# Kernel optimization log

Measured on AMD Instinct MI355X. Metric: run time of the kernel, lower is better.

Reference implementation:

```python
import jax, jax.numpy as jnp
import numpy as np

TEMPERATURE = 0.07
BASE_TEMPERATURE = 0.07


def setup_inputs() -> dict:
    key = jax.random.key(0)
    k1, k2 = jax.random.split(key)
    N, D = 8192, 512
    features = jax.random.normal(k1, (N, D), dtype=jnp.float32)
    labels = jax.random.randint(k2, (N,), 0, 64, dtype=jnp.int64 if jax.config.jax_enable_x64 else jnp.int32)
    return {"features": features, "labels": labels, "rotation_multiplier": 2}


def reference(features, labels, rotation_multiplier):
    k = int(rotation_multiplier)
    N = features.shape[0]
    B = N // k
    # L2-normalize rows (torch F.normalize clamps norm at eps=1e-12)
    norm = jnp.maximum(jnp.linalg.norm(features, axis=1, keepdims=True), 1e-12)
    f = features / norm
    sim = jnp.matmul(f, f.T) / TEMPERATURE  # [N, N]

    # block positive mask: groups of k rows share a label; compare group labels
    lab = labels.reshape(B, k)[:, 0]  # [B]
    same = lab[:, None] == lab[None, :]  # [B, B]
    mask = jnp.repeat(jnp.repeat(same, k, axis=0), k, axis=1)  # [N, N]
    eye = jnp.eye(N, dtype=bool)
    mask = mask & ~eye

    # stable masked log-softmax with diagonal removed from denominator
    logits_max = jax.lax.stop_gradient(jnp.max(sim, axis=1, keepdims=True))
    logits = sim - logits_max
    exp_logits = jnp.exp(logits)
    denom = exp_logits.sum(axis=1, keepdims=True) - jnp.diagonal(exp_logits)[:, None] + 1e-8
    log_prob = logits - jnp.log(denom)

    mask_f = mask.astype(logits.dtype)
    mask_sum = mask_f.sum(axis=1)  # [N]
    valid = mask_sum > 0
    mean_log_prob_pos = (log_prob * mask_f).sum(axis=1) / jnp.maximum(mask_sum, 1.0)
    per_sample = -(TEMPERATURE / BASE_TEMPERATURE) * mean_log_prob_pos
    n_valid = valid.sum().astype(logits.dtype)
    loss = jnp.where(valid, per_sample, 0.0).sum() / jnp.maximum(n_valid, 1.0)
    return loss
```

## Files before the change

### kernel.cpp

```cpp
#include <hip/hip_runtime.h>
#include <hip/hip_bf16.h>

#define TEMP_INV 14.285714285714286f
#define FSCALE 16.0f
#define T1S (TEMP_INV / 256.0f)

typedef __attribute__((ext_vector_type(4))) float f32x4;
typedef __attribute__((ext_vector_type(4))) int i32x4;
typedef __attribute__((ext_vector_type(8))) int i32x8;

#define ASYNC_COPY16(gp, lp)                                                  \
  __builtin_amdgcn_global_load_lds(                                          \
      (__attribute__((address_space(1))) const void*)(gp),                    \
      (__attribute__((address_space(3))) void*)(lp), 16, 0, 0)

__global__ __launch_bounds__(256) void norm_k(const float* __restrict__ feat,
                                              uchar* __restrict__ fq,
                                              const int* __restrict__ labels,
                                              const int* __restrict__ kptr,
                                              int* __restrict__ glab,
                                              float* __restrict__ gacc,
                                              int* __restrict__ dcnt,
                                              int N, int D) {
  const int row = (blockIdx.x * 256 + threadIdx.x) >> 6;
  const int lane = threadIdx.x & 63;
  if (row < N) {
    const float4* fr = (const float4*)(feat + (size_t)row * D);
    float4 v0 = fr[lane * 2];
    float4 v1 = fr[lane * 2 + 1];
    float ss = v0.x * v0.x + v0.y * v0.y + v0.z * v0.z + v0.w * v0.w +
               v1.x * v1.x + v1.y * v1.y + v1.z * v1.z + v1.w * v1.w;
    #pragma unroll
    for (int off = 32; off; off >>= 1) ss += __shfl_xor(ss, off, 64);
    const float inv = FSCALE / fmaxf(sqrtf(ss), 1e-12f);
    int w0 = 0, w1 = 0;
    w0 = __builtin_amdgcn_cvt_pk_fp8_f32(v0.x * inv, v0.y * inv, w0, false);
    w0 = __builtin_amdgcn_cvt_pk_fp8_f32(v0.z * inv, v0.w * inv, w0, true);
    w1 = __builtin_amdgcn_cvt_pk_fp8_f32(v1.x * inv, v1.y * inv, w1, false);
    w1 = __builtin_amdgcn_cvt_pk_fp8_f32(v1.z * inv, v1.w * inv, w1, true);
    uint2 o; o.x = (uint)w0; o.y = (uint)w1;
    const int pofs = (lane >> 4) * 128 + (lane & 3) * 32 + ((lane >> 2) & 3) * 8;
    *(uint2*)(fq + (size_t)row * D + pofs) = o;
    if (lane == 0) {
      const int k = *kptr;
      glab[row] = labels[(size_t)(row / k) * k];
    }
  }
  if (blockIdx.x == 0 && threadIdx.x < 3) {
    if (threadIdx.x < 2) gacc[threadIdx.x] = 0.f;
    else *dcnt = 0;
  }
}

__global__ __launch_bounds__(256, 4) void gemm_k(const uchar* __restrict__ fq,
                                                 const int* __restrict__ glab,
                                                 float* __restrict__ part,
                                                 int N, int D) {
  __shared__ uchar As[128 * 128];
  __shared__ uchar Bs[128 * 128];
  const int t = threadIdx.x;
  const int lane = t & 63;
  const int wid = t >> 6;
  const int wrow = wid >> 1, wcol = wid & 1;
  const int quad = lane >> 4, l15 = lane & 15;

  const int nb = N / 128;
  const int total = nb * (nb + 1) / 2;
  int gidx = blockIdx.x;
  if ((total & 7) == 0) {
    const int per = total >> 3;
    gidx = (blockIdx.x & 7) * per + (blockIdx.x >> 3);
  }
  int idx = gidx, bi = 0;
  while (idx >= nb - bi) { idx -= nb - bi; bi++; }
  const int bj = bi + idx;
  const int i0 = bi * 128, j0 = bj * 128;
  const bool diagblk = (bi == bj);

  f32x4 acc[4][4];
  #pragma unroll
  for (int mi = 0; mi < 4; mi++)
    #pragma unroll
    for (int ni = 0; ni < 4; ni++) {
      f32x4 z = {0.f, 0.f, 0.f, 0.f};
      acc[mi][ni] = z;
    }

  uchar* sb = (wid < 2) ? As : Bs;
  const int rbase = (wid & 1) * 64;
  const int rowstart = ((wid < 2) ? i0 : j0) + rbase;
  const int lrow = lane >> 3;
  const int lch = lane & 7;

  for (int kb = 0; kb < D; kb += 128) {
    __syncthreads();
    #pragma unroll
    for (int i = 0; i < 8; i++) {
      const int rl = 8 * i + lrow;
      const int cg = lch ^ (rl & 7);
      ASYNC_COPY16(fq + (size_t)(rowstart + rl) * D + kb + cg * 16,
                   sb + (rbase + 8 * i) * 128);
    }
    __syncthreads();
    i32x8 av[4];
    #pragma unroll
    for (int mi = 0; mi < 4; mi++) {
      const int r = wrow * 64 + mi * 16 + l15;
      i32x4 lo = *(const i32x4*)&As[r * 128 + (((2 * quad) ^ (r & 7)) << 4)];
      i32x4 hi = *(const i32x4*)&As[r * 128 + (((2 * quad + 1) ^ (r & 7)) << 4)];
      av[mi] = (i32x8){lo.x, lo.y, lo.z, lo.w, hi.x, hi.y, hi.z, hi.w};
    }
    #pragma unroll
    for (int ni = 0; ni < 4; ni++) {
      const int r = wcol * 64 + ni * 16 + l15;
      i32x4 lo = *(const i32x4*)&Bs[r * 128 + (((2 * quad) ^ (r & 7)) << 4)];
      i32x4 hi = *(const i32x4*)&Bs[r * 128 + (((2 * quad + 1) ^ (r & 7)) << 4)];
      i32x8 bv = (i32x8){lo.x, lo.y, lo.z, lo.w, hi.x, hi.y, hi.z, hi.w};
      #pragma unroll
      for (int mi = 0; mi < 4; mi++)
        acc[mi][ni] = __builtin_amdgcn_mfma_scale_f32_16x16x128_f8f6f4(
            av[mi], bv, acc[mi][ni], 0, 0, 0, 127, 0, 127);
    }
  }

  __syncthreads();
  float* sf = (float*)As;
  const int colbase = j0 + wcol * 64 + l15;
  int clab[4];
  #pragma unroll
  for (int ni = 0; ni < 4; ni++) clab[ni] = glab[colbase + ni * 16];

  float colE[4] = {0.f, 0.f, 0.f, 0.f};
  float colP[4] = {0.f, 0.f, 0.f, 0.f};

  #pragma unroll
  for (int mi = 0; mi < 4; mi++) {
    const int lrw = wrow * 64 + mi * 16 + quad * 4;
    #pragma unroll
    for (int r = 0; r < 4; r++) {
      const int row = i0 + lrw + r;
      const int rlab = glab[row];
      float Ssum = 0.f, Psum = 0.f;
      #pragma unroll
      for (int ni = 0; ni < 4; ni++) {
        const int col = colbase + ni * 16;
        const float val = acc[mi][ni][r];
        const float lg = fmaf(val, T1S, -TEMP_INV);
        const bool diag = diagblk && (row == col);
        const float e = diag ? 0.f : __expf(lg);
        const float pm = (!diag && rlab == clab[ni]) ? lg : 0.f;
        Ssum += e; Psum += pm;
        colE[ni] += e; colP[ni] += pm;
      }
      #pragma unroll
      for (int off = 8; off; off >>= 1) {
        Ssum += __shfl_xor(Ssum, off, 64);
        Psum += __shfl_xor(Psum, off, 64);
      }
      if (l15 == 0) {
        sf[wcol * 128 + lrw + r]       = Ssum;
        sf[256 + wcol * 128 + lrw + r] = Psum;
      }
    }
  }
  if (!diagblk) {
    #pragma unroll
    for (int ni = 0; ni < 4; ni++) {
      float e = colE[ni];
      float p = colP[ni];
      e += __shfl_xor(e, 16, 64);
      e += __shfl_xor(e, 32, 64);
      p += __shfl_xor(p, 16, 64);
      p += __shfl_xor(p, 32, 64);
      const int lcol = wcol * 64 + ni * 16 + l15;
      if (quad == 0) {
        sf[512 + wrow * 128 + lcol] = e;
        sf[768 + wrow * 128 + lcol] = p;
      }
    }
  }
  __syncthreads();
  float* dst = part + (size_t)gidx * 512;
  if (t < 128) {
    dst[t]       = sf[t] + sf[128 + t];
    dst[128 + t] = sf[256 + t] + sf[384 + t];
  } else if (!diagblk) {
    const int u = t - 128;
    dst[256 + u] = sf[512 + u] + sf[640 + u];
    dst[384 + u] = sf[768 + u] + sf[896 + u];
  }
}

__global__ __launch_bounds__(1024) void reduce_loss_k(const float* __restrict__ part,
                                                      const int* __restrict__ glab,
                                                      const int* __restrict__ labels,
                                                      const int* __restrict__ kptr,
                                                      float* __restrict__ gacc,
                                                      int* __restrict__ dcnt,
                                                      float* __restrict__ out, int N) {
  const int nb = N / 128;
  const int b = blockIdx.x;
  const int tt = threadIdx.x;
  const int t = tt & 127;
  const int sl = tt >> 7;
  const int k = *kptr;
  const int B = N / k;

  __shared__ int h[64];
  if (tt < 64) h[tt] = 0;
  __syncthreads();
  for (int g = tt; g < B; g += 1024) {
    int lb = labels[(size_t)g * k];
    if (lb >= 0 && lb < 64) atomicAdd(&h[lb], 1);
  }

  float S = 0.f, P = 0.f;
  const int base = b * nb - b * (b - 1) / 2;
  for (int bj = b + sl; bj < nb; bj += 8) {
    const float* p = part + (size_t)(base + bj - b) * 512;
    S += p[t];
    P += p[128 + t];
  }
  for (int bi = sl; bi < b; bi += 8) {
    const int idx = bi * nb - bi * (bi - 1) / 2 + (b - bi);
    const float* p = part + (size_t)idx * 512;
    S += p[256 + t];
    P += p[384 + t];
  }
  __shared__ float sS[8][128], sP[8][128];
  sS[sl][t] = S; sP[sl][t] = P;
  __syncthreads();
  float l = 0.f, v = 0.f;
  if (sl == 0) {
    S = 0.f; P = 0.f;
    #pragma unroll
    for (int s = 0; s < 8; s++) { S += sS[s][t]; P += sP[s][t]; }
    const int np = h[glab[b * 128 + t]] * k - 1;
    if (np > 0) {
      l = -(P - (float)np * logf(S + 1e-8f)) / (float)np;
      v = 1.f;
    }
  }
  #pragma unroll
  for (int off = 32; off; off >>= 1) {
    l += __shfl_xor(l, off, 64);
    v += __shfl_xor(v, off, 64);
  }
  __shared__ float sl16[16], sv16[16];
  if ((tt & 63) == 0) { sl16[tt >> 6] = l; sv16[tt >> 6] = v; }
  __syncthreads();
  if (tt == 0) {
    float L = 0.f, V = 0.f;
    #pragma unroll
    for (int i = 0; i < 16; i++) { L += sl16[i]; V += sv16[i]; }
    atomicAdd(&gacc[0], L);
    atomicAdd(&gacc[1], V);
    __threadfence();
    const int prev = atomicAdd(dcnt, 1);
    if (prev == (int)gridDim.x - 1) {
      const float Lf = atomicAdd(&gacc[0], 0.f);
      const float Vf = atomicAdd(&gacc[1], 0.f);
      out[0] = Lf / fmaxf(Vf, 1.f);
    }
  }
}

extern "C" void kernel_launch(void* const* d_in, const int* in_sizes, int n_in,
                              void* d_out, int out_size, void* d_ws, size_t ws_size,
                              hipStream_t stream) {
  const float* feat = (const float*)d_in[0];
  const int* labels = (const int*)d_in[1];
  const int* kptr   = (const int*)d_in[2];
  const int N = in_sizes[1];
  const int D = in_sizes[0] / N;

  const int nb = N / 128;
  const int total = nb * (nb + 1) / 2;

  char* ws = (char*)d_ws;
  uchar* fq = (uchar*)ws;
  size_t off = (size_t)N * D;
  float* part = (float*)(ws + off); off += (size_t)total * 512 * sizeof(float);
  int* glab   = (int*)(ws + off);   off += (size_t)N * sizeof(int);
  float* gacc = (float*)(ws + off); off += 2 * sizeof(float);
  int* dcnt   = (int*)(ws + off);   off += sizeof(int);

  norm_k<<<(N + 3) / 4, 256, 0, stream>>>(feat, fq, labels, kptr, glab,
                                          gacc, dcnt, N, D);
  gemm_k<<<total, 256, 0, stream>>>(fq, glab, part, N, D);
  reduce_loss_k<<<nb, 1024, 0, stream>>>(part, glab, labels, kptr, gacc, dcnt,
                                         (float*)d_out, N);
}
```

Measured before the change: 128.7 us.

## Double-buffer LDS tiles in the FP8 GEMM to overlap loads with MFMA

The single As/Bs LDS tiles become double buffers, and the next K-slice is prefetched with async global-to-LDS copies while the current slice is consumed. Manual vmcnt waits and raw barriers replace the two __syncthreads per iteration, and s_setprio raises wave priority around the MFMA block. This is meant to hide global load latency behind matrix math. It doubles LDS use to 64KB per block and drops the launch-bounds occupancy hint from 4 to 2 blocks per CU, which reduces latency hiding across blocks.

```diff
diff --git a/kernel.cpp b/kernel.cpp
--- a/kernel.cpp
+++ b/kernel.cpp
@@ -52,12 +52,12 @@
   }
 }
 
-__global__ __launch_bounds__(256, 4) void gemm_k(const uchar* __restrict__ fq,
+__global__ __launch_bounds__(256, 2) void gemm_k(const uchar* __restrict__ fq,
                                                  const int* __restrict__ glab,
                                                  float* __restrict__ part,
                                                  int N, int D) {
-  __shared__ uchar As[128 * 128];
-  __shared__ uchar Bs[128 * 128];
+  __shared__ uchar As[2][128 * 128];
+  __shared__ uchar Bs[2][128 * 128];
   const int t = threadIdx.x;
   const int lane = t & 63;
   const int wid = t >> 6;
@@ -86,44 +86,59 @@
       acc[mi][ni] = z;
     }
 
-  uchar* sb = (wid < 2) ? As : Bs;
   const int rbase = (wid & 1) * 64;
   const int rowstart = ((wid < 2) ? i0 : j0) + rbase;
   const int lrow = lane >> 3;
   const int lch = lane & 7;
-
-  for (int kb = 0; kb < D; kb += 128) {
-    __syncthreads();
+  const uchar* gsrc = fq + (size_t)rowstart * D;
+
+  auto STAGE = [&](int buf, int kbyte) {
+    uchar* sb = (wid < 2) ? As[buf] : Bs[buf];
     #pragma unroll
     for (int i = 0; i < 8; i++) {
       const int rl = 8 * i + lrow;
       const int cg = lch ^ (rl & 7);
-      ASYNC_COPY16(fq + (size_t)(rowstart + rl) * D + kb + cg * 16,
+      ASYNC_COPY16(gsrc + (size_t)rl * D + kbyte + cg * 16,
                    sb + (rbase + 8 * i) * 128);
     }
-    __syncthreads();
+  };
+
+  const int nk = D >> 7;
+  STAGE(0, 0);
+  for (int kt = 0; kt < nk; kt++) {
+    const int cur = kt & 1;
+    if (kt + 1 < nk) {
+      STAGE(cur ^ 1, (kt + 1) << 7);
+      asm volatile("s_waitcnt vmcnt(8)" ::: "memory");
+    } else {
+      asm volatile("s_waitcnt vmcnt(0)" ::: "memory");
+    }
+    asm volatile("s_barrier" ::: "memory");
+
     i32x8 av[4];
     #pragma unroll
     for (int mi = 0; mi < 4; mi++) {
       const int r = wrow * 64 + mi * 16 + l15;
-      i32x4 lo = *(const i32x4*)&As[r * 128 + (((2 * quad) ^ (r & 7)) << 4)];
-      i32x4 hi = *(const i32x4*)&As[r * 128 + (((2 * quad + 1) ^ (r & 7)) << 4)];
+      i32x4 lo = *(const i32x4*)&As[cur][r * 128 + (((2 * quad) ^ (r & 7)) << 4)];
+      i32x4 hi = *(const i32x4*)&As[cur][r * 128 + (((2 * quad + 1) ^ (r & 7)) << 4)];
       av[mi] = (i32x8){lo.x, lo.y, lo.z, lo.w, hi.x, hi.y, hi.z, hi.w};
     }
+    __builtin_amdgcn_s_setprio(1);
     #pragma unroll
     for (int ni = 0; ni < 4; ni++) {
       const int r = wcol * 64 + ni * 16 + l15;
-      i32x4 lo = *(const i32x4*)&Bs[r * 128 + (((2 * quad) ^ (r & 7)) << 4)];
-      i32x4 hi = *(const i32x4*)&Bs[r * 128 + (((2 * quad + 1) ^ (r & 7)) << 4)];
+      i32x4 lo = *(const i32x4*)&Bs[cur][r * 128 + (((2 * quad) ^ (r & 7)) << 4)];
+      i32x4 hi = *(const i32x4*)&Bs[cur][r * 128 + (((2 * quad + 1) ^ (r & 7)) << 4)];
       i32x8 bv = (i32x8){lo.x, lo.y, lo.z, lo.w, hi.x, hi.y, hi.z, hi.w};
       #pragma unroll
       for (int mi = 0; mi < 4; mi++)
         acc[mi][ni] = __builtin_amdgcn_mfma_scale_f32_16x16x128_f8f6f4(
             av[mi], bv, acc[mi][ni], 0, 0, 0, 127, 0, 127);
     }
-  }
-
-  __syncthreads();
+    __builtin_amdgcn_s_setprio(0);
+    asm volatile("s_barrier" ::: "memory");
+  }
+
   float* sf = (float*)As;
   const int colbase = j0 + wcol * 64 + l15;
   int clab[4];
```

Measured after the change: 130.7 us. About the same (+1.6%).

## Load FP8 MFMA operands directly from global memory, dropping LDS staging

Applied to the files above, without the earlier changes.

The GEMM no longer stages A and B tiles in LDS through async global-to-LDS copies with barriers. Each wave now reads its MFMA operand fragments straight from global memory, relying on cache for reuse, and fully unrolls the K loop when D is 512. LDS shrinks to a small float scratch for the epilogue and launch bounds drop to 2 blocks per CU, giving more registers. The cost is redundant global and L2 traffic, since waves sharing rows each fetch their own copy, and the loads become uncoalesced 16-byte row fragments.

```diff
diff --git a/kernel.cpp b/kernel.cpp
--- a/kernel.cpp
+++ b/kernel.cpp
@@ -8,11 +8,6 @@
 typedef __attribute__((ext_vector_type(4))) float f32x4;
 typedef __attribute__((ext_vector_type(4))) int i32x4;
 typedef __attribute__((ext_vector_type(8))) int i32x8;
-
-#define ASYNC_COPY16(gp, lp)                                                  \
-  __builtin_amdgcn_global_load_lds(                                          \
-      (__attribute__((address_space(1))) const void*)(gp),                    \
-      (__attribute__((address_space(3))) void*)(lp), 16, 0, 0)
 
 __global__ __launch_bounds__(256) void norm_k(const float* __restrict__ feat,
                                               uchar* __restrict__ fq,
@@ -52,12 +47,11 @@
   }
 }
 
-__global__ __launch_bounds__(256, 4) void gemm_k(const uchar* __restrict__ fq,
+__global__ __launch_bounds__(256, 2) void gemm_k(const uchar* __restrict__ fq,
                                                  const int* __restrict__ glab,
                                                  float* __restrict__ part,
                                                  int N, int D) {
-  __shared__ uchar As[128 * 128];
-  __shared__ uchar Bs[128 * 128];
+  __shared__ float sf[1024];
   const int t = threadIdx.x;
   const int lane = t & 63;
   const int wid = t >> 6;
@@ -86,45 +80,43 @@
       acc[mi][ni] = z;
     }
 
-  uchar* sb = (wid < 2) ? As : Bs;
-  const int rbase = (wid & 1) * 64;
-  const int rowstart = ((wid < 2) ? i0 : j0) + rbase;
-  const int lrow = lane >> 3;
-  const int lch = lane & 7;
-
-  for (int kb = 0; kb < D; kb += 128) {
-    __syncthreads();
-    #pragma unroll
-    for (int i = 0; i < 8; i++) {
-      const int rl = 8 * i + lrow;
-      const int cg = lch ^ (rl & 7);
-      ASYNC_COPY16(fq + (size_t)(rowstart + rl) * D + kb + cg * 16,
-                   sb + (rbase + 8 * i) * 128);
-    }
-    __syncthreads();
-    i32x8 av[4];
-    #pragma unroll
-    for (int mi = 0; mi < 4; mi++) {
-      const int r = wrow * 64 + mi * 16 + l15;
-      i32x4 lo = *(const i32x4*)&As[r * 128 + (((2 * quad) ^ (r & 7)) << 4)];
-      i32x4 hi = *(const i32x4*)&As[r * 128 + (((2 * quad + 1) ^ (r & 7)) << 4)];
-      av[mi] = (i32x8){lo.x, lo.y, lo.z, lo.w, hi.x, hi.y, hi.z, hi.w};
-    }
-    #pragma unroll
-    for (int ni = 0; ni < 4; ni++) {
-      const int r = wcol * 64 + ni * 16 + l15;
-      i32x4 lo = *(const i32x4*)&Bs[r * 128 + (((2 * quad) ^ (r & 7)) << 4)];
-      i32x4 hi = *(const i32x4*)&Bs[r * 128 + (((2 * quad + 1) ^ (r & 7)) << 4)];
-      i32x8 bv = (i32x8){lo.x, lo.y, lo.z, lo.w, hi.x, hi.y, hi.z, hi.w};
-      #pragma unroll
-      for (int mi = 0; mi < 4; mi++)
-        acc[mi][ni] = __builtin_amdgcn_mfma_scale_f32_16x16x128_f8f6f4(
-            av[mi], bv, acc[mi][ni], 0, 0, 0, 127, 0, 127);
-    }
-  }
-
-  __syncthreads();
-  float* sf = (float*)As;
+  const uchar* ap[4];
+  const uchar* bp[4];
+  #pragma unroll
+  for (int mi = 0; mi < 4; mi++)
+    ap[mi] = fq + (size_t)(i0 + wrow * 64 + mi * 16 + l15) * D + quad * 32;
+  #pragma unroll
+  for (int ni = 0; ni < 4; ni++)
+    bp[ni] = fq + (size_t)(j0 + wcol * 64 + ni * 16 + l15) * D + quad * 32;
+
+#define KSTEP(kb)                                                             \
+  {                                                                           \
+    i32x8 bv[4];                                                              \
+    _Pragma("unroll")                                                         \
+    for (int ni = 0; ni < 4; ni++) {                                          \
+      i32x4 lo = *(const i32x4*)(bp[ni] + (kb));                              \
+      i32x4 hi = *(const i32x4*)(bp[ni] + (kb) + 16);                         \
+      bv[ni] = (i32x8){lo.x, lo.y, lo.z, lo.w, hi.x, hi.y, hi.z, hi.w};       \
+    }                                                                         \
+    _Pragma("unroll")                                                         \
+    for (int mi = 0; mi < 4; mi++) {                                          \
+      i32x4 lo = *(const i32x4*)(ap[mi] + (kb));                              \
+      i32x4 hi = *(const i32x4*)(ap[mi] + (kb) + 16);                         \
+      i32x8 av = (i32x8){lo.x, lo.y, lo.z, lo.w, hi.x, hi.y, hi.z, hi.w};     \
+      _Pragma("unroll")                                                       \
+      for (int ni = 0; ni < 4; ni++)                                          \
+        acc[mi][ni] = __builtin_amdgcn_mfma_scale_f32_16x16x128_f8f6f4(       \
+            av, bv[ni], acc[mi][ni], 0, 0, 0, 127, 0, 127);                   \
+    }                                                                         \
+  }
+
+  if (D == 512) {
+    KSTEP(0) KSTEP(128) KSTEP(256) KSTEP(384)
+  } else {
+    for (int kb = 0; kb < D; kb += 128) KSTEP(kb)
+  }
+#undef KSTEP
+
   const int colbase = j0 + wcol * 64 + l15;
   int clab[4];
   #pragma unroll
```

After: 160.7 us. 24.9% more time.
